# Kernel optimization log

Hardware: AMD Instinct MI355X
Metric: run time of the kernel (lower is better)

Reference implementation:

```python
import jax, jax.numpy as jnp
import numpy as np

NT, NC, E = 50, 20, 64   # n_types, n_categories, embedding_size
B, L = 4, 256            # batch, seq_len
TIME_SCALE = 100.0


def setup_inputs() -> dict:
    key = jax.random.key(0)
    ks = jax.random.split(key, 12)
    times = jnp.sort(jax.random.uniform(ks[0], (B, L), dtype=jnp.float32) * TIME_SCALE, axis=1)
    types = jax.random.randint(ks[1], (B, L), 0, NT)
    cats = jax.random.randint(ks[2], (B, L), 0, NC)
    p = lambda k, s: 0.1 * jax.random.normal(k, s, dtype=jnp.float32)
    # type_emb / a positively biased so intensity stays > 0 (log is taken on it)
    type_emb = 0.05 * jax.random.normal(ks[3], (NT, E), dtype=jnp.float32) + 0.1
    a = 0.1 * jnp.abs(jax.random.normal(ks[5], (NT, E), dtype=jnp.float32)) + 0.2
    return {
        "event_times": times,
        "event_types": types,
        "event_categories": cats,
        "T": 128,
        "type_emb": type_emb,
        "cat_emb": p(ks[4], (NC, E)),
        "a": a,
        "b": p(ks[6], (NC, E)),
        "A": p(ks[7], (NT, NT, E)),
        "P": p(ks[8], (NT, NT, E)),
        "Bm": p(ks[9], (NC, NC, E)),
        "Q": p(ks[10], (NC, NC, E)),
    }


def _intensity(type_emb, cat_emb, a, b, A, P, Bm, Q, times, types, cats, hist_len, t_now):
    """Intensity over all event types given history times[:hist_len]. Returns [NT]."""
    Lr = times.shape[0]
    mask = jnp.arange(Lr) < hist_len                       # [L]
    td = jnp.where(mask, t_now - times, 0.0)               # [L]
    # --- type channel: m[t,e] = sum_s f[t]*A[k_s,t]*exp(-f[t]*P[k_s,t]*f[k_s]*td_s)*f[k_s]
    f_eth = type_emb[types]                                # [L,E]
    decay = jnp.exp(-(type_emb[None] * P[types]) * f_eth[:, None, :] * td[:, None, None])  # [L,NT,E]
    contrib = type_emb[None] * A[types] * decay * f_eth[:, None, :]
    m = jnp.sum(jnp.where(mask[:, None, None], contrib, 0.0), axis=0)   # [NT,E]
    # --- category channel: n[c,e] analogous with g/B/Q
    g_eth = cat_emb[cats]                                  # [L,E]
    cdecay = jnp.exp(-(cat_emb[None] * Q[cats]) * g_eth[:, None, :] * td[:, None, None])  # [L,NC,E]
    ccontrib = cat_emb[None] * Bm[cats] * cdecay * g_eth[:, None, :]
    n = jnp.sum(jnp.where(mask[:, None, None], ccontrib, 0.0), axis=0)  # [NC,E]
    last_cat = cats[jnp.maximum(hist_len - 1, 0)]          # cats[-1] of the history
    base = type_emb * a                                    # [NT,E]
    full = jnp.sum(base + type_emb * b[last_cat][None] + m + type_emb * n[last_cat][None], axis=1)
    empty = jnp.sum(jax.nn.softplus(base), axis=1)         # empty-history branch
    return jnp.where(hist_len == 0, empty, full)           # [NT]


def reference(event_times, event_types, event_categories, T, type_emb, cat_emb, a, b, A, P, Bm, Q):
    Tf = jnp.float32(T)
    Lr = event_times.shape[1]
    inten = lambda ts, ty, ct, h, tn: _intensity(type_emb, cat_emb, a, b, A, P, Bm, Q, ts, ty, ct, h, tn)

    def per_seq(times, types, cats):
        def step(ll, i):
            lam_vec = inten(times, types, cats, i, times[i])
            lam = lam_vec[types[i]]
            c = jnp.where(times[i] >= 0, jnp.log(lam + 1e-16) + lam, 0.0)
            return ll + c, None
        ll, _ = jax.lax.scan(step, jnp.float32(0.0), jnp.arange(Lr))
        total_int = inten(times, types, cats, Lr, Tf)       # intensity at horizon T, full history
        I0 = jnp.sum(jax.nn.softplus(type_emb * a))         # empty-history intensity summed over types
        integral = jnp.sum(total_int) * (Tf - times[-1]) + I0 * times[0]
        return ll, integral

    lls, ints = jax.vmap(per_seq)(event_times, event_types, event_categories)
    return -(jnp.sum(lls) - jnp.sum(ints))
```

## Files before the change

### kernel.cpp

```cpp
#include <hip/hip_runtime.h>

#define NTYPES 50
#define NCATS  20
#define EDIM   64
#define BATCH  4
#define SEQL   256

#define LL_BLOCKS 512
#define IT_BLOCKS 200
#define IC_BLOCKS 4
#define TOTAL_BLOCKS 717

#define SLOT(tgt, g) (((tgt) * 16 + (g)) * 32)
#define SUBC(g)      ((96 + (g)) * 32)
#define TOPC         (112 * 32)
#define WS_ZERO_BYTES ((112 * 32 + 1) * 4)

__device__ __forceinline__ float softplusf(float x) {
    return (x > 0.f) ? x + log1pf(__expf(-x)) : log1pf(__expf(x));
}

__device__ __forceinline__ float waveReduceSum(float v) {
    #pragma unroll
    for (int off = 32; off > 0; off >>= 1) v += __shfl_down(v, off, 64);
    return v;
}

__global__ __launch_bounds__(256) void hawkes_fused(
        const float* __restrict__ times,
        const int*   __restrict__ types,
        const int*   __restrict__ cats,
        const int*   __restrict__ Tp,
        const float* __restrict__ type_emb,
        const float* __restrict__ cat_emb,
        const float* __restrict__ amat,
        const float* __restrict__ bmat,
        const float* __restrict__ A,
        const float* __restrict__ P,
        const float* __restrict__ Bm,
        const float* __restrict__ Q,
        float* __restrict__ ws,
        float* __restrict__ out) {
    const int blk  = blockIdx.x;
    const int tid  = threadIdx.x;
    const int lane = tid & 63;
    const int wave = tid >> 6;
    const int g    = blk & 15;

    __shared__ float red1[4], red2[4];
    __shared__ float sn[4][EDIM];
    __shared__ float fin[96];
    __shared__ int   finflag;

    if (blk < LL_BLOCKS) {
        const int b  = blk >> 7;
        const int pr = blk & 127;
        const int i1 = pr, i2 = 255 - pr;
        const int base = b * SEQL;
        const int t1 = types[base + i1], t2 = types[base + i2];
        const int c2 = cats[base + i2 - 1];
        const int c1 = (i1 > 0) ? cats[base + i1 - 1] : 0;
        const float te1 = type_emb[t1 * EDIM + lane];
        const float te2 = type_emb[t2 * EDIM + lane];
        const float ce1 = cat_emb[c1 * EDIM + lane];
        const float ce2 = cat_emb[c2 * EDIM + lane];
        const float ti1 = times[base + i1], ti2 = times[base + i2];

        float acc1 = 0.f, acc2 = 0.f;
        #pragma unroll 4
        for (int s = wave; s < i1; s += 4) {
            const int   k  = types[base + s];
            const int   cs = cats [base + s];
            const float ts = times[base + s];
            const float f  = type_emb[k  * EDIM + lane];
            const float gg = cat_emb [cs * EDIM + lane];
            const float A1 = A [(k  * NTYPES + t1) * EDIM + lane];
            const float P1 = P [(k  * NTYPES + t1) * EDIM + lane];
            const float B1 = Bm[(cs * NCATS  + c1) * EDIM + lane];
            const float Q1 = Q [(cs * NCATS  + c1) * EDIM + lane];
            const float A2 = A [(k  * NTYPES + t2) * EDIM + lane];
            const float P2 = P [(k  * NTYPES + t2) * EDIM + lane];
            const float B2 = Bm[(cs * NCATS  + c2) * EDIM + lane];
            const float Q2 = Q [(cs * NCATS  + c2) * EDIM + lane];
            const float td1 = ti1 - ts, td2 = ti2 - ts;
            const float tf1 = te1 * f, cg1 = ce1 * gg;
            const float tf2 = te2 * f, cg2 = ce2 * gg;
            acc1 += tf1 * A1 * __expf(-tf1 * P1 * td1) + cg1 * B1 * __expf(-cg1 * Q1 * td1);
            acc2 += tf2 * A2 * __expf(-tf2 * P2 * td2) + cg2 * B2 * __expf(-cg2 * Q2 * td2);
        }
        const int n1 = (i1 > wave) ? ((i1 - wave + 3) >> 2) : 0;
        #pragma unroll 4
        for (int s = wave + 4 * n1; s < i2; s += 4) {
            const int   k  = types[base + s];
            const int   cs = cats [base + s];
            const float ts = times[base + s];
            const float f  = type_emb[k  * EDIM + lane];
            const float gg = cat_emb [cs * EDIM + lane];
            const float A2 = A [(k  * NTYPES + t2) * EDIM + lane];
            const float P2 = P [(k  * NTYPES + t2) * EDIM + lane];
            const float B2 = Bm[(cs * NCATS  + c2) * EDIM + lane];
            const float Q2 = Q [(cs * NCATS  + c2) * EDIM + lane];
            const float td2 = ti2 - ts;
            const float tf2 = te2 * f, cg2 = ce2 * gg;
            acc2 += tf2 * A2 * __expf(-tf2 * P2 * td2) + cg2 * B2 * __expf(-cg2 * Q2 * td2);
        }
        if (wave == 0) {
            if (i1 == 0) acc1 += softplusf(te1 * amat[t1 * EDIM + lane]);
            else         acc1 += te1 * (amat[t1 * EDIM + lane] + bmat[c1 * EDIM + lane]);
        } else if (wave == 1) {
            acc2 += te2 * (amat[t2 * EDIM + lane] + bmat[c2 * EDIM + lane]);
        }
        const float r1 = waveReduceSum(acc1);
        const float r2 = waveReduceSum(acc2);
        if (lane == 0) { red1[wave] = r1; red2[wave] = r2; }
        __syncthreads();
        if (tid == 0) {
            const float lam1 = red1[0] + red1[1] + red1[2] + red1[3];
            const float lam2 = red2[0] + red2[1] + red2[2] + red2[3];
            atomicAdd(&ws[SLOT(0, g)], logf(lam1 + 1e-16f) + lam1
                                     + logf(lam2 + 1e-16f) + lam2);
        }
    } else if (blk < LL_BLOCKS + IT_BLOCKS) {
        const int bt = blk - LL_BLOCKS;
        const int b = bt / NTYPES, t = bt % NTYPES;
        const int base = b * SEQL;
        const float Tf = (float)Tp[0];
        const float te = type_emb[t * EDIM + lane];
        float acc = 0.f;
        #pragma unroll 4
        for (int s = wave; s < SEQL; s += 4) {
            const int   k  = types[base + s];
            const float td = Tf - times[base + s];
            const float f  = type_emb[k * EDIM + lane];
            const float Ak = A[(k * NTYPES + t) * EDIM + lane];
            const float Pk = P[(k * NTYPES + t) * EDIM + lane];
            const float tf = te * f;
            acc += tf * Ak * __expf(-tf * Pk * td);
        }
        const float r = waveReduceSum(acc);
        if (lane == 0) red1[wave] = r;
        __syncthreads();
        if (tid == 0)
            atomicAdd(&ws[SLOT(1 + b, g)], red1[0] + red1[1] + red1[2] + red1[3]);
    } else if (blk < LL_BLOCKS + IT_BLOCKS + IC_BLOCKS) {
        const int b = blk - LL_BLOCKS - IT_BLOCKS;
        const int base = b * SEQL;
        const float Tf = (float)Tp[0];
        const int   lc = cats[base + SEQL - 1];
        const float ce = cat_emb[lc * EDIM + lane];
        float nacc = 0.f;
        #pragma unroll 4
        for (int s = wave; s < SEQL; s += 4) {
            const int   cs = cats[base + s];
            const float td = Tf - times[base + s];
            const float gg = cat_emb[cs * EDIM + lane];
            const float Bk = Bm[(cs * NCATS + lc) * EDIM + lane];
            const float Qk = Q [(cs * NCATS + lc) * EDIM + lane];
            const float cg = ce * gg;
            nacc += cg * Bk * __expf(-cg * Qk * td);
        }
        sn[wave][lane] = nacc;
        __syncthreads();
        if (wave == 0) {
            const float n_e = sn[0][lane] + sn[1][lane] + sn[2][lane] + sn[3][lane];
            float TA = 0.f, TS = 0.f;
            for (int t = 0; t < NTYPES; ++t) {
                const float tv = type_emb[t * EDIM + lane];
                TA += tv * amat[t * EDIM + lane];
                TS += tv;
            }
            float term = TA + (bmat[lc * EDIM + lane] + n_e) * TS;
            term = waveReduceSum(term);
            if (lane == 0) atomicAdd(&ws[SLOT(1 + b, g)], term);
        }
    } else {
        float acc = 0.f;
        for (int t = wave; t < NTYPES; t += 4)
            acc += softplusf(type_emb[t * EDIM + lane] * amat[t * EDIM + lane]);
        const float r = waveReduceSum(acc);
        if (lane == 0) red1[wave] = r;
        __syncthreads();
        if (tid == 0)
            atomicAdd(&ws[SLOT(5, g)], red1[0] + red1[1] + red1[2] + red1[3]);
    }

    if (tid == 0) {
        finflag = 0;
        __asm__ __volatile__("s_waitcnt vmcnt(0)" ::: "memory");
        const unsigned cnt_g = (unsigned)((TOTAL_BLOCKS + 15 - g) >> 4);
        unsigned old = atomicAdd((unsigned int*)&ws[SUBC(g)], 1u);
        if (old == cnt_g - 1u) {
            unsigned o2 = atomicAdd((unsigned int*)&ws[TOPC], 1u);
            if (o2 == 15u) finflag = 1;
        }
    }
    __syncthreads();
    if (finflag) {
        if (tid < 96) fin[tid] = atomicAdd(&ws[tid * 32], 0.f);
        __syncthreads();
        if (tid == 0) {
            float ll = 0.f, i0 = 0.f;
            for (int j = 0; j < 16; ++j) { ll += fin[j]; i0 += fin[80 + j]; }
            const float Tf = (float)Tp[0];
            float tot = 0.f;
            for (int b2 = 0; b2 < BATCH; ++b2) {
                float ib = 0.f;
                for (int j = 0; j < 16; ++j) ib += fin[(1 + b2) * 16 + j];
                tot += ib * (Tf - times[b2 * SEQL + SEQL - 1]) + i0 * times[b2 * SEQL];
            }
            out[0] = -(ll - tot);
        }
    }
}

extern "C" void kernel_launch(void* const* d_in, const int* in_sizes, int n_in,
                              void* d_out, int out_size, void* d_ws, size_t ws_size,
                              hipStream_t stream) {
    const float* times    = (const float*)d_in[0];
    const int*   types    = (const int*)  d_in[1];
    const int*   cats     = (const int*)  d_in[2];
    const int*   Tp       = (const int*)  d_in[3];
    const float* type_emb = (const float*)d_in[4];
    const float* cat_emb  = (const float*)d_in[5];
    const float* amat     = (const float*)d_in[6];
    const float* bmat     = (const float*)d_in[7];
    const float* A        = (const float*)d_in[8];
    const float* P        = (const float*)d_in[9];
    const float* Bm       = (const float*)d_in[10];
    const float* Q        = (const float*)d_in[11];
    float* out = (float*)d_out;
    float* ws  = (float*)d_ws;

    hipMemsetAsync(ws, 0, WS_ZERO_BYTES, stream);

    hawkes_fused<<<TOTAL_BLOCKS, 256, 0, stream>>>(times, types, cats, Tp,
                                                   type_emb, cat_emb, amat, bmat,
                                                   A, P, Bm, Q, ws, out);
}
```

Before: 99.88 us.

## Factor exponential decay into prefix sums per target and split final reduction kernel

The decay term exp(-R*(tau-ts)) is factored as exp(-R*tau)*exp(R*ts), so each block, one per (batch, target type or category), streams the sequence once. It builds running per-source sums in shared memory and evaluates the intensity only at events whose type or previous category matches its target. This replaces the old O(L^2) per-event history scans full of global gathers with roughly O(L) work plus a small per-event reduction. The memset and grid-wide atomic completion counter give way to a second single-block kernel that does the final log-likelihood and integral reduction. The cost is a sequential, barrier-heavy loop over matching events, shared-memory atomics, and possible overflow or precision loss in exp(R*ts) if the decay rates or times were larger.

```diff
diff --git a/kernel.cpp b/kernel.cpp
--- a/kernel.cpp
+++ b/kernel.cpp
@@ -1,20 +1,19 @@
 #include <hip/hip_runtime.h>
 
-#define NTYPES 50
-#define NCATS  20
-#define EDIM   64
-#define BATCH  4
-#define SEQL   256
-
-#define LL_BLOCKS 512
-#define IT_BLOCKS 200
-#define IC_BLOCKS 4
-#define TOTAL_BLOCKS 717
-
-#define SLOT(tgt, g) (((tgt) * 16 + (g)) * 32)
-#define SUBC(g)      ((96 + (g)) * 32)
-#define TOPC         (112 * 32)
-#define WS_ZERO_BYTES ((112 * 32 + 1) * 4)
+#define NTY 50
+#define NCA 20
+#define ED  64
+#define NB  4
+#define SL  256
+
+#define TYPE_BLOCKS (NB * NTY)
+#define CAT_BLOCKS  (NB * NCA)
+#define MAIN_BLOCKS (TYPE_BLOCKS + CAT_BLOCKS)
+
+#define WS_M  0
+#define WS_N  (NB * SL)
+#define WS_IT (2 * NB * SL)
+#define WS_NT (2 * NB * SL + NB * NTY)
 
 __device__ __forceinline__ float softplusf(float x) {
     return (x > 0.f) ? x + log1pf(__expf(-x)) : log1pf(__expf(x));
@@ -26,7 +25,7 @@
     return v;
 }
 
-__global__ __launch_bounds__(256) void hawkes_fused(
+__global__ __launch_bounds__(256) void hawkes_main(
         const float* __restrict__ times,
         const int*   __restrict__ types,
         const int*   __restrict__ cats,
@@ -39,177 +38,180 @@
         const float* __restrict__ P,
         const float* __restrict__ Bm,
         const float* __restrict__ Q,
-        float* __restrict__ ws,
-        float* __restrict__ out) {
+        float* __restrict__ ws) {
     const int blk  = blockIdx.x;
     const int tid  = threadIdx.x;
     const int lane = tid & 63;
-    const int wave = tid >> 6;
-    const int g    = blk & 15;
-
-    __shared__ float red1[4], red2[4];
-    __shared__ float sn[4][EDIM];
-    __shared__ float fin[96];
-    __shared__ int   finflag;
-
-    if (blk < LL_BLOCKS) {
-        const int b  = blk >> 7;
-        const int pr = blk & 127;
-        const int i1 = pr, i2 = 255 - pr;
-        const int base = b * SEQL;
-        const int t1 = types[base + i1], t2 = types[base + i2];
-        const int c2 = cats[base + i2 - 1];
-        const int c1 = (i1 > 0) ? cats[base + i1 - 1] : 0;
-        const float te1 = type_emb[t1 * EDIM + lane];
-        const float te2 = type_emb[t2 * EDIM + lane];
-        const float ce1 = cat_emb[c1 * EDIM + lane];
-        const float ce2 = cat_emb[c2 * EDIM + lane];
-        const float ti1 = times[base + i1], ti2 = times[base + i2];
-
-        float acc1 = 0.f, acc2 = 0.f;
+    const int w    = tid >> 6;
+
+    const bool isType = blk < TYPE_BLOCKS;
+    const int  b   = isType ? blk / NTY : (blk - TYPE_BLOCKS) / NCA;
+    const int  tgt = isType ? blk % NTY : (blk - TYPE_BLOCKS) % NCA;
+    const int  NK  = isType ? NTY : NCA;
+    const int  base = b * SL;
+
+    __shared__ float Wk[NTY * ED];
+    __shared__ float Rk[NTY * ED];
+    __shared__ float Ck[NTY * ED];
+    __shared__ float times_sh[SL + 1];
+    __shared__ int   types_sh[SL];
+    __shared__ int   cats_sh[SL];
+    __shared__ float qp[4][ED];
+    __shared__ int   evl[SL];
+    __shared__ int   evcnt;
+
+    times_sh[tid] = times[base + tid];
+    types_sh[tid] = types[base + tid];
+    cats_sh[tid]  = cats[base + tid];
+    if (tid == 0) times_sh[SL] = (float)Tp[0];
+    __syncthreads();
+
+    const float tr   = isType ? type_emb[tgt * ED + lane] : cat_emb[tgt * ED + lane];
+    const float areg = isType ? amat[tgt * ED + lane] : 0.f;
+
+    for (int k = w; k < NK; k += 4) {
+        float f, Cv, Pv;
+        if (isType) {
+            f  = type_emb[k * ED + lane];
+            Cv = A[(k * NTY + tgt) * ED + lane];
+            Pv = P[(k * NTY + tgt) * ED + lane];
+        } else {
+            f  = cat_emb[k * ED + lane];
+            Cv = Bm[(k * NCA + tgt) * ED + lane];
+            Pv = Q [(k * NCA + tgt) * ED + lane];
+        }
+        Ck[k * ED + lane] = tr * Cv * f;
+        Rk[k * ED + lane] = tr * Pv * f;
+        Wk[k * ED + lane] = 0.f;
+    }
+
+    if (w == 0) {
+        int run = 0;
+        #pragma unroll
+        for (int jj = 0; jj < 4; ++jj) {
+            const int p = lane + 64 * jj;
+            const bool pred = (p >= 1) && (isType ? (types_sh[p] == tgt)
+                                                  : (cats_sh[p - 1] == tgt));
+            const unsigned long long mk = __ballot(pred);
+            if (pred) evl[run + __popcll(mk & ((1ull << lane) - 1ull))] = p;
+            run += __popcll(mk);
+        }
+        if (lane == 0) evcnt = run;
+    }
+    __syncthreads();
+
+    const int ne = evcnt;
+    int prev = 0;
+    for (int j = 0; j <= ne; ++j) {
+        const int ie = (j < ne) ? evl[j] : SL;
+
+        float evrow = 0.f;
+        if (w == 0 && j < ne) {
+            evrow = isType ? bmat[cats_sh[ie - 1] * ED + lane]
+                           : type_emb[types_sh[ie] * ED + lane];
+        }
+
         #pragma unroll 4
-        for (int s = wave; s < i1; s += 4) {
-            const int   k  = types[base + s];
-            const int   cs = cats [base + s];
-            const float ts = times[base + s];
-            const float f  = type_emb[k  * EDIM + lane];
-            const float gg = cat_emb [cs * EDIM + lane];
-            const float A1 = A [(k  * NTYPES + t1) * EDIM + lane];
-            const float P1 = P [(k  * NTYPES + t1) * EDIM + lane];
-            const float B1 = Bm[(cs * NCATS  + c1) * EDIM + lane];
-            const float Q1 = Q [(cs * NCATS  + c1) * EDIM + lane];
-            const float A2 = A [(k  * NTYPES + t2) * EDIM + lane];
-            const float P2 = P [(k  * NTYPES + t2) * EDIM + lane];
-            const float B2 = Bm[(cs * NCATS  + c2) * EDIM + lane];
-            const float Q2 = Q [(cs * NCATS  + c2) * EDIM + lane];
-            const float td1 = ti1 - ts, td2 = ti2 - ts;
-            const float tf1 = te1 * f, cg1 = ce1 * gg;
-            const float tf2 = te2 * f, cg2 = ce2 * gg;
-            acc1 += tf1 * A1 * __expf(-tf1 * P1 * td1) + cg1 * B1 * __expf(-cg1 * Q1 * td1);
-            acc2 += tf2 * A2 * __expf(-tf2 * P2 * td2) + cg2 * B2 * __expf(-cg2 * Q2 * td2);
-        }
-        const int n1 = (i1 > wave) ? ((i1 - wave + 3) >> 2) : 0;
-        #pragma unroll 4
-        for (int s = wave + 4 * n1; s < i2; s += 4) {
-            const int   k  = types[base + s];
-            const int   cs = cats [base + s];
-            const float ts = times[base + s];
-            const float f  = type_emb[k  * EDIM + lane];
-            const float gg = cat_emb [cs * EDIM + lane];
-            const float A2 = A [(k  * NTYPES + t2) * EDIM + lane];
-            const float P2 = P [(k  * NTYPES + t2) * EDIM + lane];
-            const float B2 = Bm[(cs * NCATS  + c2) * EDIM + lane];
-            const float Q2 = Q [(cs * NCATS  + c2) * EDIM + lane];
-            const float td2 = ti2 - ts;
-            const float tf2 = te2 * f, cg2 = ce2 * gg;
-            acc2 += tf2 * A2 * __expf(-tf2 * P2 * td2) + cg2 * B2 * __expf(-cg2 * Q2 * td2);
-        }
-        if (wave == 0) {
-            if (i1 == 0) acc1 += softplusf(te1 * amat[t1 * EDIM + lane]);
-            else         acc1 += te1 * (amat[t1 * EDIM + lane] + bmat[c1 * EDIM + lane]);
-        } else if (wave == 1) {
-            acc2 += te2 * (amat[t2 * EDIM + lane] + bmat[c2 * EDIM + lane]);
-        }
-        const float r1 = waveReduceSum(acc1);
-        const float r2 = waveReduceSum(acc2);
-        if (lane == 0) { red1[wave] = r1; red2[wave] = r2; }
+        for (int s = prev + w; s < ie; s += 4) {
+            const int k = isType ? types_sh[s] : cats_sh[s];
+            atomicAdd(&Wk[k * ED + lane], __expf(Rk[k * ED + lane] * times_sh[s]));
+        }
         __syncthreads();
-        if (tid == 0) {
-            const float lam1 = red1[0] + red1[1] + red1[2] + red1[3];
-            const float lam2 = red2[0] + red2[1] + red2[2] + red2[3];
-            atomicAdd(&ws[SLOT(0, g)], logf(lam1 + 1e-16f) + lam1
-                                     + logf(lam2 + 1e-16f) + lam2);
-        }
-    } else if (blk < LL_BLOCKS + IT_BLOCKS) {
-        const int bt = blk - LL_BLOCKS;
-        const int b = bt / NTYPES, t = bt % NTYPES;
-        const int base = b * SEQL;
-        const float Tf = (float)Tp[0];
-        const float te = type_emb[t * EDIM + lane];
-        float acc = 0.f;
-        #pragma unroll 4
-        for (int s = wave; s < SEQL; s += 4) {
-            const int   k  = types[base + s];
-            const float td = Tf - times[base + s];
-            const float f  = type_emb[k * EDIM + lane];
-            const float Ak = A[(k * NTYPES + t) * EDIM + lane];
-            const float Pk = P[(k * NTYPES + t) * EDIM + lane];
-            const float tf = te * f;
-            acc += tf * Ak * __expf(-tf * Pk * td);
-        }
-        const float r = waveReduceSum(acc);
-        if (lane == 0) red1[wave] = r;
+
+        const float tau = times_sh[ie];
+        float q = 0.f;
+        for (int k = w; k < NK; k += 4)
+            q += Ck[k * ED + lane] * __expf(-Rk[k * ED + lane] * tau) * Wk[k * ED + lane];
+        qp[w][lane] = q;
         __syncthreads();
-        if (tid == 0)
-            atomicAdd(&ws[SLOT(1 + b, g)], red1[0] + red1[1] + red1[2] + red1[3]);
-    } else if (blk < LL_BLOCKS + IT_BLOCKS + IC_BLOCKS) {
-        const int b = blk - LL_BLOCKS - IT_BLOCKS;
-        const int base = b * SEQL;
-        const float Tf = (float)Tp[0];
-        const int   lc = cats[base + SEQL - 1];
-        const float ce = cat_emb[lc * EDIM + lane];
-        float nacc = 0.f;
-        #pragma unroll 4
-        for (int s = wave; s < SEQL; s += 4) {
-            const int   cs = cats[base + s];
-            const float td = Tf - times[base + s];
-            const float gg = cat_emb[cs * EDIM + lane];
-            const float Bk = Bm[(cs * NCATS + lc) * EDIM + lane];
-            const float Qk = Q [(cs * NCATS + lc) * EDIM + lane];
-            const float cg = ce * gg;
-            nacc += cg * Bk * __expf(-cg * Qk * td);
-        }
-        sn[wave][lane] = nacc;
+
+        if (w == 0) {
+            const float qs = qp[0][lane] + qp[1][lane] + qp[2][lane] + qp[3][lane];
+            if (isType) {
+                if (j < ne) {
+                    const float v = waveReduceSum(qs + tr * (areg + evrow));
+                    if (lane == 0) ws[WS_M + b * SL + ie] = v;
+                } else {
+                    const float v = waveReduceSum(qs + tr * areg);
+                    if (lane == 0) ws[WS_IT + b * NTY + tgt] = v;
+                }
+            } else {
+                if (j < ne) {
+                    const float v = waveReduceSum(qs * evrow);
+                    if (lane == 0) ws[WS_N + b * SL + ie] = v;
+                } else if (tgt == cats_sh[SL - 1]) {
+                    ws[WS_NT + b * ED + lane] = qs;
+                }
+            }
+        }
         __syncthreads();
-        if (wave == 0) {
-            const float n_e = sn[0][lane] + sn[1][lane] + sn[2][lane] + sn[3][lane];
-            float TA = 0.f, TS = 0.f;
-            for (int t = 0; t < NTYPES; ++t) {
-                const float tv = type_emb[t * EDIM + lane];
-                TA += tv * amat[t * EDIM + lane];
-                TS += tv;
-            }
-            float term = TA + (bmat[lc * EDIM + lane] + n_e) * TS;
-            term = waveReduceSum(term);
-            if (lane == 0) atomicAdd(&ws[SLOT(1 + b, g)], term);
-        }
-    } else {
-        float acc = 0.f;
-        for (int t = wave; t < NTYPES; t += 4)
-            acc += softplusf(type_emb[t * EDIM + lane] * amat[t * EDIM + lane]);
-        const float r = waveReduceSum(acc);
-        if (lane == 0) red1[wave] = r;
-        __syncthreads();
-        if (tid == 0)
-            atomicAdd(&ws[SLOT(5, g)], red1[0] + red1[1] + red1[2] + red1[3]);
-    }
+        prev = ie;
+    }
+}
+
+__global__ __launch_bounds__(256) void hawkes_final(
+        const float* __restrict__ times,
+        const int*   __restrict__ types,
+        const int*   __restrict__ cats,
+        const int*   __restrict__ Tp,
+        const float* __restrict__ type_emb,
+        const float* __restrict__ amat,
+        const float* __restrict__ bmat,
+        const float* __restrict__ ws,
+        float* __restrict__ out) {
+    const int tid  = threadIdx.x;
+    const int lane = tid & 63;
+    const int w    = tid >> 6;
+
+    __shared__ float tsl[4][ED];
+    __shared__ float wred[4], i0red[4], intb[4];
+
+    const float Tf = (float)Tp[0];
+
+    float llp = 0.f;
+    const int i = tid + 1;
+    if (i < SL) {
+        #pragma unroll
+        for (int bb = 0; bb < NB; ++bb) {
+            const float lam = ws[WS_M + bb * SL + i] + ws[WS_N + bb * SL + i];
+            llp += logf(lam + 1e-16f) + lam;
+        }
+    }
+
+    const int t0 = types[w * SL];
+    const float v0 = softplusf(type_emb[t0 * ED + lane] * amat[t0 * ED + lane]);
+
+    float tsp = 0.f, i0p = 0.f;
+    for (int t = w; t < NTY; t += 4) {
+        const float tv = type_emb[t * ED + lane];
+        tsp += tv;
+        i0p += softplusf(tv * amat[t * ED + lane]);
+    }
+    tsl[w][lane] = tsp;
+
+    const float lam0 = waveReduceSum(v0);
+    const float wll  = waveReduceSum(llp);
+    const float wi0  = waveReduceSum(i0p);
+    if (lane == 0) {
+        wred[w]  = wll + logf(lam0 + 1e-16f) + lam0;
+        i0red[w] = wi0;
+    }
+    __syncthreads();
+
+    const float TS_l = tsl[0][lane] + tsl[1][lane] + tsl[2][lane] + tsl[3][lane];
+    const int   lc   = cats[w * SL + SL - 1];
+    const float bbv  = bmat[lc * ED + lane] + ws[WS_NT + w * ED + lane];
+    const float its  = (lane < NTY) ? ws[WS_IT + w * NTY + lane] : 0.f;
+    const float ip   = waveReduceSum(its + bbv * TS_l);
+    if (lane == 0) intb[w] = ip * (Tf - times[w * SL + SL - 1]);
+    __syncthreads();
 
     if (tid == 0) {
-        finflag = 0;
-        __asm__ __volatile__("s_waitcnt vmcnt(0)" ::: "memory");
-        const unsigned cnt_g = (unsigned)((TOTAL_BLOCKS + 15 - g) >> 4);
-        unsigned old = atomicAdd((unsigned int*)&ws[SUBC(g)], 1u);
-        if (old == cnt_g - 1u) {
-            unsigned o2 = atomicAdd((unsigned int*)&ws[TOPC], 1u);
-            if (o2 == 15u) finflag = 1;
-        }
-    }
-    __syncthreads();
-    if (finflag) {
-        if (tid < 96) fin[tid] = atomicAdd(&ws[tid * 32], 0.f);
-        __syncthreads();
-        if (tid == 0) {
-            float ll = 0.f, i0 = 0.f;
-            for (int j = 0; j < 16; ++j) { ll += fin[j]; i0 += fin[80 + j]; }
-            const float Tf = (float)Tp[0];
-            float tot = 0.f;
-            for (int b2 = 0; b2 < BATCH; ++b2) {
-                float ib = 0.f;
-                for (int j = 0; j < 16; ++j) ib += fin[(1 + b2) * 16 + j];
-                tot += ib * (Tf - times[b2 * SEQL + SEQL - 1]) + i0 * times[b2 * SEQL];
-            }
-            out[0] = -(ll - tot);
-        }
+        const float ll = wred[0] + wred[1] + wred[2] + wred[3];
+        const float I0 = i0red[0] + i0red[1] + i0red[2] + i0red[3];
+        const float t0s = times[0] + times[SL] + times[2 * SL] + times[3 * SL];
+        const float tot = intb[0] + intb[1] + intb[2] + intb[3] + I0 * t0s;
+        out[0] = -(ll - tot);
     }
 }
 
@@ -231,9 +233,9 @@
     float* out = (float*)d_out;
     float* ws  = (float*)d_ws;
 
-    hipMemsetAsync(ws, 0, WS_ZERO_BYTES, stream);
-
-    hawkes_fused<<<TOTAL_BLOCKS, 256, 0, stream>>>(times, types, cats, Tp,
-                                                   type_emb, cat_emb, amat, bmat,
-                                                   A, P, Bm, Q, ws, out);
-}
+    hawkes_main<<<MAIN_BLOCKS, 256, 0, stream>>>(times, types, cats, Tp,
+                                                 type_emb, cat_emb, amat, bmat,
+                                                 A, P, Bm, Q, ws);
+    hawkes_final<<<1, 256, 0, stream>>>(times, types, cats, Tp,
+                                        type_emb, amat, bmat, ws, out);
+}
```

Measured after the change: 149.5 us. 49.7% more time.

## Precompute combined coefficient tables in a prep kernel to cut per-event gathers

Applied to the files above, without the earlier changes.

Adds a build_tables kernel that folds type_emb/cat_emb products into A/P and Bm/Q. It writes interleaved float2 tables (amplitude, decay rate) to workspace. The main kernel then does one float2 gather per channel instead of separate embedding, A and P loads plus multiplies. This lowers memory traffic and ALU work in the hot loops, at the cost of an extra kernel launch and writing about 1.3 MB of tables on every call.

```diff
diff --git a/kernel.cpp b/kernel.cpp
--- a/kernel.cpp
+++ b/kernel.cpp
@@ -16,6 +16,11 @@
 #define TOPC         (112 * 32)
 #define WS_ZERO_BYTES ((112 * 32 + 1) * 4)
 
+#define TBL_T_OFF 65536
+#define NT_ELEMS  (NTYPES * NTYPES * EDIM)
+#define NC_ELEMS  (NCATS * NCATS * EDIM)
+#define TBL_C_OFF (TBL_T_OFF + 2 * NT_ELEMS)
+
 __device__ __forceinline__ float softplusf(float x) {
     return (x > 0.f) ? x + log1pf(__expf(-x)) : log1pf(__expf(x));
 }
@@ -24,6 +29,32 @@
     #pragma unroll
     for (int off = 32; off > 0; off >>= 1) v += __shfl_down(v, off, 64);
     return v;
+}
+
+__global__ __launch_bounds__(256) void build_tables(
+        const float* __restrict__ type_emb,
+        const float* __restrict__ cat_emb,
+        const float* __restrict__ A,
+        const float* __restrict__ P,
+        const float* __restrict__ Bm,
+        const float* __restrict__ Q,
+        float2* __restrict__ CRt,
+        float2* __restrict__ CRc) {
+    const int i = blockIdx.x * 256 + threadIdx.x;
+    if (i < NT_ELEMS) {
+        const int e = i & 63, kt = i >> 6;
+        const int t = kt % NTYPES, k = kt / NTYPES;
+        const float te = type_emb[t * EDIM + e];
+        const float f  = type_emb[k * EDIM + e];
+        CRt[i] = make_float2(te * A[i] * f, te * P[i] * f);
+    } else if (i < NT_ELEMS + NC_ELEMS) {
+        const int j = i - NT_ELEMS;
+        const int e = j & 63, kc = j >> 6;
+        const int c = kc % NCATS, k2 = kc / NCATS;
+        const float ce = cat_emb[c * EDIM + e];
+        const float g  = cat_emb[k2 * EDIM + e];
+        CRc[j] = make_float2(ce * Bm[j] * g, ce * Q[j] * g);
+    }
 }
 
 __global__ __launch_bounds__(256) void hawkes_fused(
@@ -35,10 +66,8 @@
         const float* __restrict__ cat_emb,
         const float* __restrict__ amat,
         const float* __restrict__ bmat,
-        const float* __restrict__ A,
-        const float* __restrict__ P,
-        const float* __restrict__ Bm,
-        const float* __restrict__ Q,
+        const float2* __restrict__ CRt,
+        const float2* __restrict__ CRc,
         float* __restrict__ ws,
         float* __restrict__ out) {
     const int blk  = blockIdx.x;
@@ -60,10 +89,6 @@
         const int t1 = types[base + i1], t2 = types[base + i2];
         const int c2 = cats[base + i2 - 1];
         const int c1 = (i1 > 0) ? cats[base + i1 - 1] : 0;
-        const float te1 = type_emb[t1 * EDIM + lane];
-        const float te2 = type_emb[t2 * EDIM + lane];
-        const float ce1 = cat_emb[c1 * EDIM + lane];
-        const float ce2 = cat_emb[c2 * EDIM + lane];
         const float ti1 = times[base + i1], ti2 = times[base + i2];
 
         float acc1 = 0.f, acc2 = 0.f;
@@ -72,21 +97,13 @@
             const int   k  = types[base + s];
             const int   cs = cats [base + s];
             const float ts = times[base + s];
-            const float f  = type_emb[k  * EDIM + lane];
-            const float gg = cat_emb [cs * EDIM + lane];
-            const float A1 = A [(k  * NTYPES + t1) * EDIM + lane];
-            const float P1 = P [(k  * NTYPES + t1) * EDIM + lane];
-            const float B1 = Bm[(cs * NCATS  + c1) * EDIM + lane];
-            const float Q1 = Q [(cs * NCATS  + c1) * EDIM + lane];
-            const float A2 = A [(k  * NTYPES + t2) * EDIM + lane];
-            const float P2 = P [(k  * NTYPES + t2) * EDIM + lane];
-            const float B2 = Bm[(cs * NCATS  + c2) * EDIM + lane];
-            const float Q2 = Q [(cs * NCATS  + c2) * EDIM + lane];
+            const float2 t1v = CRt[(k  * NTYPES + t1) * EDIM + lane];
+            const float2 t2v = CRt[(k  * NTYPES + t2) * EDIM + lane];
+            const float2 c1v = CRc[(cs * NCATS  + c1) * EDIM + lane];
+            const float2 c2v = CRc[(cs * NCATS  + c2) * EDIM + lane];
             const float td1 = ti1 - ts, td2 = ti2 - ts;
-            const float tf1 = te1 * f, cg1 = ce1 * gg;
-            const float tf2 = te2 * f, cg2 = ce2 * gg;
-            acc1 += tf1 * A1 * __expf(-tf1 * P1 * td1) + cg1 * B1 * __expf(-cg1 * Q1 * td1);
-            acc2 += tf2 * A2 * __expf(-tf2 * P2 * td2) + cg2 * B2 * __expf(-cg2 * Q2 * td2);
+            acc1 += t1v.x * __expf(-t1v.y * td1) + c1v.x * __expf(-c1v.y * td1);
+            acc2 += t2v.x * __expf(-t2v.y * td2) + c2v.x * __expf(-c2v.y * td2);
         }
         const int n1 = (i1 > wave) ? ((i1 - wave + 3) >> 2) : 0;
         #pragma unroll 4
@@ -94,20 +111,17 @@
             const int   k  = types[base + s];
             const int   cs = cats [base + s];
             const float ts = times[base + s];
-            const float f  = type_emb[k  * EDIM + lane];
-            const float gg = cat_emb [cs * EDIM + lane];
-            const float A2 = A [(k  * NTYPES + t2) * EDIM + lane];
-            const float P2 = P [(k  * NTYPES + t2) * EDIM + lane];
-            const float B2 = Bm[(cs * NCATS  + c2) * EDIM + lane];
-            const float Q2 = Q [(cs * NCATS  + c2) * EDIM + lane];
+            const float2 t2v = CRt[(k  * NTYPES + t2) * EDIM + lane];
+            const float2 c2v = CRc[(cs * NCATS  + c2) * EDIM + lane];
             const float td2 = ti2 - ts;
-            const float tf2 = te2 * f, cg2 = ce2 * gg;
-            acc2 += tf2 * A2 * __expf(-tf2 * P2 * td2) + cg2 * B2 * __expf(-cg2 * Q2 * td2);
+            acc2 += t2v.x * __expf(-t2v.y * td2) + c2v.x * __expf(-c2v.y * td2);
         }
         if (wave == 0) {
+            const float te1 = type_emb[t1 * EDIM + lane];
             if (i1 == 0) acc1 += softplusf(te1 * amat[t1 * EDIM + lane]);
             else         acc1 += te1 * (amat[t1 * EDIM + lane] + bmat[c1 * EDIM + lane]);
         } else if (wave == 1) {
+            const float te2 = type_emb[t2 * EDIM + lane];
             acc2 += te2 * (amat[t2 * EDIM + lane] + bmat[c2 * EDIM + lane]);
         }
         const float r1 = waveReduceSum(acc1);
@@ -125,17 +139,13 @@
         const int b = bt / NTYPES, t = bt % NTYPES;
         const int base = b * SEQL;
         const float Tf = (float)Tp[0];
-        const float te = type_emb[t * EDIM + lane];
         float acc = 0.f;
         #pragma unroll 4
         for (int s = wave; s < SEQL; s += 4) {
             const int   k  = types[base + s];
             const float td = Tf - times[base + s];
-            const float f  = type_emb[k * EDIM + lane];
-            const float Ak = A[(k * NTYPES + t) * EDIM + lane];
-            const float Pk = P[(k * NTYPES + t) * EDIM + lane];
-            const float tf = te * f;
-            acc += tf * Ak * __expf(-tf * Pk * td);
+            const float2 v = CRt[(k * NTYPES + t) * EDIM + lane];
+            acc += v.x * __expf(-v.y * td);
         }
         const float r = waveReduceSum(acc);
         if (lane == 0) red1[wave] = r;
@@ -147,17 +157,13 @@
         const int base = b * SEQL;
         const float Tf = (float)Tp[0];
         const int   lc = cats[base + SEQL - 1];
-        const float ce = cat_emb[lc * EDIM + lane];
         float nacc = 0.f;
         #pragma unroll 4
         for (int s = wave; s < SEQL; s += 4) {
             const int   cs = cats[base + s];
             const float td = Tf - times[base + s];
-            const float gg = cat_emb[cs * EDIM + lane];
-            const float Bk = Bm[(cs * NCATS + lc) * EDIM + lane];
-            const float Qk = Q [(cs * NCATS + lc) * EDIM + lane];
-            const float cg = ce * gg;
-            nacc += cg * Bk * __expf(-cg * Qk * td);
+            const float2 v = CRc[(cs * NCATS + lc) * EDIM + lane];
+            nacc += v.x * __expf(-v.y * td);
         }
         sn[wave][lane] = nacc;
         __syncthreads();
@@ -231,9 +237,16 @@
     float* out = (float*)d_out;
     float* ws  = (float*)d_ws;
 
+    float2* CRt = (float2*)(ws + TBL_T_OFF);
+    float2* CRc = (float2*)(ws + TBL_C_OFF);
+
     hipMemsetAsync(ws, 0, WS_ZERO_BYTES, stream);
+
+    const int tbl_blocks = (NT_ELEMS + NC_ELEMS + 255) / 256;
+    build_tables<<<tbl_blocks, 256, 0, stream>>>(type_emb, cat_emb,
+                                                 A, P, Bm, Q, CRt, CRc);
 
     hawkes_fused<<<TOTAL_BLOCKS, 256, 0, stream>>>(times, types, cats, Tp,
                                                    type_emb, cat_emb, amat, bmat,
-                                                   A, P, Bm, Q, ws, out);
-}
+                                                   CRt, CRc, ws, out);
+}
```

Result: no change. 98.50 us (-1.4%).
